# Optimization experiments

Measured on AMD Instinct MI355X. Metric: run time of the kernel, lower is better.

Reference implementation:

```python
import jax, jax.numpy as jnp
import numpy as np

N = 100000   # nodes
E = 1600000  # edges (avg degree 16)
F = 64       # num_features
H = 32       # hidden_size
C = 2        # num_classes
BN_EPS = 1e-5


def setup_inputs() -> dict:
    key = jax.random.key(0)
    ks = jax.random.split(key, 16)
    s_in = 1.0 / np.sqrt(F)
    s_h = 1.0 / np.sqrt(H)
    s_l = 1.0 / np.sqrt(3 * H)
    return {
        "x": jax.random.normal(ks[0], (N, F), jnp.float32),
        "edge_index": jax.random.randint(ks[1], (2, E), 0, N, dtype=jnp.int32),
        "edge_weights": jax.random.uniform(ks[2], (E,), jnp.float32),
        # GCNConv 1
        "W1": jax.random.uniform(ks[3], (F, H), jnp.float32, -s_in, s_in),
        "b1": jnp.zeros((H,), jnp.float32),
        "g1": jnp.ones((H,), jnp.float32),
        "be1": jnp.zeros((H,), jnp.float32),
        # GCNConv 2
        "W2": jax.random.uniform(ks[4], (H, H), jnp.float32, -s_h, s_h),
        "b2": jnp.zeros((H,), jnp.float32),
        "g2": jnp.ones((H,), jnp.float32),
        "be2": jnp.zeros((H,), jnp.float32),
        # GCNConv 3
        "W3": jax.random.uniform(ks[5], (H, H), jnp.float32, -s_h, s_h),
        "b3": jnp.zeros((H,), jnp.float32),
        "g3": jnp.ones((H,), jnp.float32),
        "be3": jnp.zeros((H,), jnp.float32),
        # Final linear: (3H -> C)
        "Wl": jax.random.uniform(ks[6], (3 * H, C), jnp.float32, -s_l, s_l),
        "bl": jax.random.uniform(ks[7], (C,), jnp.float32, -s_l, s_l),
    }


def _gcn_conv(x, W, b, row, col, w, n):
    # PyG GCNConv: h = x @ W; symmetric normalization with self-loops; scatter-add; + bias
    h = x @ W                                            # [N, H]
    deg = jax.ops.segment_sum(w, col, num_segments=n)    # [N]
    dis = jnp.where(deg > 0, jax.lax.rsqrt(deg), 0.0)    # deg^{-1/2}
    norm = dis[row] * w * dis[col]                       # [E+N]
    msg = h[row] * norm[:, None]                         # gather + normalize
    out = jax.ops.segment_sum(msg, col, num_segments=n)  # scatter-add to targets
    return out + b


def _bn(x, gamma, beta):
    # BatchNorm1d with batch statistics (biased variance), affine
    mu = x.mean(axis=0)
    var = x.var(axis=0)
    return (x - mu) * jax.lax.rsqrt(var + BN_EPS) * gamma + beta


def reference(x, edge_index, edge_weights,
              W1, b1, g1, be1,
              W2, b2, g2, be2,
              W3, b3, g3, be3,
              Wl, bl):
    n = x.shape[0]
    loops = jnp.arange(n, dtype=edge_index.dtype)
    row = jnp.concatenate([edge_index[0], loops])        # sources + self-loops
    col = jnp.concatenate([edge_index[1], loops])        # targets + self-loops
    w = jnp.concatenate([edge_weights, jnp.ones((n,), edge_weights.dtype)])

    out1 = _bn(jax.nn.relu(_gcn_conv(x, W1, b1, row, col, w, n)), g1, be1)
    out2 = _bn(jax.nn.relu(_gcn_conv(out1, W2, b2, row, col, w, n)), g2, be2)
    out3 = _bn(jax.nn.relu(_gcn_conv(out2, W3, b3, row, col, w, n)), g3, be3)

    rep = jnp.concatenate([out1, out2, out3], axis=1)    # [N, 3H]
    return rep @ Wl + bl                                 # [N, C]
```

## Files before the change

kernel.cpp:

```cpp
#include <hip/hip_runtime.h>

typedef unsigned int uint;
typedef unsigned char uchar;
typedef unsigned short ushort;
typedef unsigned long long ull;

#define F_IN 64
#define HD 32
#define NCLS 2
#define BN_EPS 1e-5f
#define SCHUNK 1024
#define NCOPY 8
#define FIX_SCALE 1073741824.0f
#define FIX_INV   9.313225746154785e-10f
#define MASK40 ((1ULL << 40) - 1)

__device__ __forceinline__ ull ld64(const int2* p) {
    return *reinterpret_cast<const ull*>(p);
}
__device__ __forceinline__ ushort f2bf(float f) {
    uint u = __float_as_uint(f);
    u = (u + 0x7FFFu + ((u >> 16) & 1u)) >> 16;
    return (ushort)u;
}
__device__ __forceinline__ float bf2f(ushort b) {
    return __uint_as_float((uint)b << 16);
}
__device__ __forceinline__ uchar f2e4(float x) {
    uint u = __float_as_uint(x);
    uint s = u & 0x80000000u;
    uint mag = u & 0x7fffffffu;
    if (mag < 0x3c800000u) return (uchar)(s >> 24);
    if (mag > 0x43e00000u) mag = 0x43e00000u;
    uint r = mag + 0x000FFFFFu + ((mag >> 20) & 1u);
    if (r > 0x43e00000u) r = 0x43e00000u;
    uint E = r >> 23;
    return (uchar)((s >> 24) | ((E - 120u) << 3) | ((r >> 20) & 7u));
}
__device__ __forceinline__ float e42f(uchar b) {
    uint s = ((uint)b & 0x80u) << 24;
    uint rest = (uint)b & 0x7fu;
    return __uint_as_float(s | ((rest << 20) + 0x3c000000u));
}

__global__ void hist64_kernel(const int* __restrict__ ei, const float* __restrict__ w,
                              ull* __restrict__ packed8, ushort* __restrict__ epos,
                              int E, int n) {
    int e = blockIdx.x * blockDim.x + threadIdx.x;
    if (e >= E) return;
    int k = blockIdx.x & (NCOPY - 1);
    int c = ei[E + e];
    ull fx = (ull)(w[e] * FIX_SCALE + 0.5f);
    ull old = atomicAdd(&packed8[(size_t)k * n + c], (1ULL << 40) | fx);
    epos[e] = (ushort)(old >> 40);
}

__global__ void scanA_kernel(const ull* __restrict__ packed8,
                             int* __restrict__ partial, float* __restrict__ dis, int n) {
    __shared__ int red[256];
    int base = blockIdx.x * SCHUNK;
    int tid = threadIdx.x;
    int s = 0;
    for (int i = tid; i < SCHUNK; i += 256) {
        int idx = base + i;
        if (idx < n) {
            int cnt = 0;
            ull fxs = 0;
#pragma unroll
            for (int k = 0; k < NCOPY; k++) {
                ull p = packed8[(size_t)k * n + idx];
                cnt += (int)(p >> 40);
                fxs += (p & MASK40);
            }
            s += cnt;
            float deg = (float)fxs * FIX_INV;
            dis[idx] = rsqrtf(deg + 1.0f);
        }
    }
    red[tid] = s;
    __syncthreads();
    for (int off = 128; off > 0; off >>= 1) {
        if (tid < off) red[tid] += red[tid + off];
        __syncthreads();
    }
    if (tid == 0) partial[blockIdx.x] = red[0];
}

__global__ void scanB_kernel(int* __restrict__ partial, int nb, int* __restrict__ offs_n) {
    __shared__ int lds[256];
    int tid = threadIdx.x;
    int v = (tid < nb) ? partial[tid] : 0;
    lds[tid] = v;
    __syncthreads();
    for (int off = 1; off < 256; off <<= 1) {
        int t = (tid >= off) ? lds[tid - off] : 0;
        __syncthreads();
        lds[tid] += t;
        __syncthreads();
    }
    if (tid < nb) partial[tid] = lds[tid] - v;
    if (tid == nb - 1) *offs_n = lds[tid];
}

__global__ void scanC_kernel(const ull* __restrict__ packed8, const int* __restrict__ partial,
                             int* __restrict__ offs, int* __restrict__ base8, int n) {
    __shared__ int lds[256];
    int tid = threadIdx.x;
    int i0 = blockIdx.x * SCHUNK + tid * 4;
    int cnt[4][NCOPY];
    int tot[4] = {0, 0, 0, 0};
#pragma unroll
    for (int t = 0; t < 4; t++) {
        int idx = i0 + t;
#pragma unroll
        for (int k = 0; k < NCOPY; k++) {
            int c = (idx < n) ? (int)(packed8[(size_t)k * n + idx] >> 40) : 0;
            cnt[t][k] = c;
            tot[t] += c;
        }
    }
    int tsum = tot[0] + tot[1] + tot[2] + tot[3];
    lds[tid] = tsum;
    __syncthreads();
    for (int off = 1; off < 256; off <<= 1) {
        int t = (tid >= off) ? lds[tid - off] : 0;
        __syncthreads();
        lds[tid] += t;
        __syncthreads();
    }
    int run = partial[blockIdx.x] + lds[tid] - tsum;
#pragma unroll
    for (int t = 0; t < 4; t++) {
        int idx = i0 + t;
        if (idx < n) {
            offs[idx] = run;
            int b = run;
#pragma unroll
            for (int k = 0; k < NCOPY; k++) {
                base8[(size_t)idx * NCOPY + k] = b;
                b += cnt[t][k];
            }
            run = b;
        }
    }
}

__global__ void fill_gemm1_kernel(const int* __restrict__ ei, const float* __restrict__ w,
                                  const int* __restrict__ base8, const ushort* __restrict__ epos,
                                  int2* __restrict__ centry, int E, int eb,
                                  const float* __restrict__ X, const float* __restrict__ W,
                                  const float* __restrict__ dis, ushort* __restrict__ Hb,
                                  float* __restrict__ statsCur, int n) {
    if ((int)blockIdx.x < eb) {
        int e = blockIdx.x * blockDim.x + threadIdx.x;
        if (e >= E) return;
        int k = blockIdx.x & (NCOPY - 1);
        int r = ei[e], c = ei[E + e];
        int pos = base8[(size_t)c * NCOPY + k] + (int)epos[e];
        centry[pos] = make_int2(r, __float_as_int(w[e]));
        return;
    }
    __shared__ float Wl[F_IN * HD];
    int gb = (int)blockIdx.x - eb;
    for (int i = threadIdx.x; i < F_IN * HD; i += blockDim.x) Wl[i] = W[i];
    if (gb == 0) {
        for (int i = threadIdx.x; i < NCOPY * 64; i += blockDim.x) statsCur[i] = 0.0f;
    }
    __syncthreads();
    int idx = gb * (int)blockDim.x + (int)threadIdx.x;
    if (idx >= n * HD) return;
    int node = idx >> 5, h = idx & 31;
    const float4* xr4 = reinterpret_cast<const float4*>(X + (size_t)node * F_IN);
    float acc = 0.0f;
#pragma unroll
    for (int q = 0; q < F_IN / 4; q++) {
        float4 v4 = xr4[q];
        float vs[4] = {v4.x, v4.y, v4.z, v4.w};
#pragma unroll
        for (int j = 0; j < 4; j++) {
            acc += vs[j] * Wl[(q * 4 + j) * HD + h];
        }
    }
    Hb[idx] = f2bf(acc * dis[node]);
}

template <bool FP8>
__global__ void gemm_bn_kernel(const float* __restrict__ X, const float* __restrict__ W,
                               const float* __restrict__ statsPrev, const float* __restrict__ g,
                               const float* __restrict__ be, const float* __restrict__ dis,
                               ushort* __restrict__ Hb, uchar* __restrict__ Hb8,
                               float* __restrict__ statsCur, int n) {
    __shared__ float Wl[HD * HD];
    __shared__ float scl[64];
    for (int i = threadIdx.x; i < HD * HD; i += blockDim.x) Wl[i] = W[i];
    if (threadIdx.x < 32) {
        int h = threadIdx.x;
        float sm = 0.f, sq = 0.f;
#pragma unroll
        for (int k = 0; k < NCOPY; k++) {
            sm += statsPrev[k * 64 + h];
            sq += statsPrev[k * 64 + 32 + h];
        }
        float invn = 1.0f / (float)n;
        float mean = sm * invn;
        float var = sq * invn - mean * mean;
        float sca = rsqrtf(var + BN_EPS) * g[h];
        scl[h] = sca;
        scl[32 + h] = be[h] - mean * sca;
    }
    if (blockIdx.x == 0) {
        for (int i = threadIdx.x; i < NCOPY * 64; i += blockDim.x) statsCur[i] = 0.0f;
    }
    __syncthreads();
    int idx = blockIdx.x * blockDim.x + threadIdx.x;
    if (idx >= n * HD) return;
    int node = idx >> 5, h = idx & 31;
    const float4* xr4 = reinterpret_cast<const float4*>(X + (size_t)node * HD);
    float acc = 0.0f;
#pragma unroll
    for (int q = 0; q < HD / 4; q++) {
        float4 v4 = xr4[q];
        float vs[4] = {v4.x, v4.y, v4.z, v4.w};
#pragma unroll
        for (int j = 0; j < 4; j++) {
            int k = q * 4 + j;
            acc += (vs[j] * scl[k] + scl[32 + k]) * Wl[k * HD + h];
        }
    }
    float v = acc * dis[node];
    if (FP8) Hb8[idx] = f2e4(v * 16.0f);
    else     Hb[idx]  = f2bf(v);
}

template <int NPW>
__global__ void aggV4n_kernel(const ushort* __restrict__ hb, const int* __restrict__ offs,
                              const int2* __restrict__ centry, const float* __restrict__ dis,
                              const float* __restrict__ bias, float* __restrict__ y,
                              float* __restrict__ stats, int n) {
    int wave = threadIdx.x >> 6, lane = threadIdx.x & 63, sub = lane >> 5, h = lane & 31;
    float bv = bias[h];
    float lsum = 0.f, lsq = 0.f;
    int base = (blockIdx.x * 4 + wave) * NPW;
    for (int t = 0; t < NPW; t++) {
        int node = base + t;
        if (node >= n) break;
        int s = offs[node], e2 = offs[node + 1];
        int len = e2 - s;
        int half = (len + 1) >> 1;
        int j    = sub ? (s + half) : s;
        int jend = sub ? e2 : (s + half);
        float dd = dis[node];
        float a0 = 0.f, a1 = 0.f, a2 = 0.f, a3 = 0.f;
        if (sub == 0) a0 = bf2f(hb[(size_t)node * HD + h]);
        for (; j + 3 < jend; j += 4) {
            ull p0 = ld64(centry + j);
            ull p1 = ld64(centry + j + 1);
            ull p2 = ld64(centry + j + 2);
            ull p3 = ld64(centry + j + 3);
            a0 += bf2f(hb[(size_t)(uint)p0 * HD + h]) * __uint_as_float((uint)(p0 >> 32));
            a1 += bf2f(hb[(size_t)(uint)p1 * HD + h]) * __uint_as_float((uint)(p1 >> 32));
            a2 += bf2f(hb[(size_t)(uint)p2 * HD + h]) * __uint_as_float((uint)(p2 >> 32));
            a3 += bf2f(hb[(size_t)(uint)p3 * HD + h]) * __uint_as_float((uint)(p3 >> 32));
        }
        for (; j < jend; j++) {
            ull p0 = ld64(centry + j);
            a0 += bf2f(hb[(size_t)(uint)p0 * HD + h]) * __uint_as_float((uint)(p0 >> 32));
        }
        a0 += a1 + a2 + a3;
        a0 += __shfl_xor(a0, 32, 64);
        float yv = fmaxf(fmaf(a0, dd, bv), 0.f);
        if (sub == 0) {
            y[(size_t)node * HD + h] = yv;
            lsum += yv; lsq += yv * yv;
        }
    }
    __shared__ float ls[4][32], lq[4][32];
    if (sub == 0) { ls[wave][h] = lsum; lq[wave][h] = lsq; }
    __syncthreads();
    if (threadIdx.x < 32) {
        int k = blockIdx.x & (NCOPY - 1);
        float a = ls[0][threadIdx.x] + ls[1][threadIdx.x] + ls[2][threadIdx.x] + ls[3][threadIdx.x];
        float b = lq[0][threadIdx.x] + lq[1][threadIdx.x] + lq[2][threadIdx.x] + lq[3][threadIdx.x];
        atomicAdd(&stats[k * 64 + threadIdx.x], a);
        atomicAdd(&stats[k * 64 + 32 + threadIdx.x], b);
    }
}

template <int NPW>
__global__ void aggV4n8_kernel(const uchar* __restrict__ hb8, const int* __restrict__ offs,
                               const int2* __restrict__ centry, const float* __restrict__ dis,
                               const float* __restrict__ bias, float* __restrict__ y,
                               float* __restrict__ stats, int n) {
    int wave = threadIdx.x >> 6, lane = threadIdx.x & 63, sub = lane >> 5, h = lane & 31;
    float bv = bias[h];
    float lsum = 0.f, lsq = 0.f;
    int base = (blockIdx.x * 4 + wave) * NPW;
    for (int t = 0; t < NPW; t++) {
        int node = base + t;
        if (node >= n) break;
        int s = offs[node], e2 = offs[node + 1];
        int len = e2 - s;
        int half = (len + 1) >> 1;
        int j    = sub ? (s + half) : s;
        int jend = sub ? e2 : (s + half);
        float dd = dis[node] * 0.0625f;
        float a0 = 0.f, a1 = 0.f, a2 = 0.f, a3 = 0.f;
        if (sub == 0) a0 = e42f(hb8[(size_t)node * HD + h]);
        for (; j + 3 < jend; j += 4) {
            ull p0 = ld64(centry + j);
            ull p1 = ld64(centry + j + 1);
            ull p2 = ld64(centry + j + 2);
            ull p3 = ld64(centry + j + 3);
            a0 += e42f(hb8[(size_t)(uint)p0 * HD + h]) * __uint_as_float((uint)(p0 >> 32));
            a1 += e42f(hb8[(size_t)(uint)p1 * HD + h]) * __uint_as_float((uint)(p1 >> 32));
            a2 += e42f(hb8[(size_t)(uint)p2 * HD + h]) * __uint_as_float((uint)(p2 >> 32));
            a3 += e42f(hb8[(size_t)(uint)p3 * HD + h]) * __uint_as_float((uint)(p3 >> 32));
        }
        for (; j < jend; j++) {
            ull p0 = ld64(centry + j);
            a0 += e42f(hb8[(size_t)(uint)p0 * HD + h]) * __uint_as_float((uint)(p0 >> 32));
        }
        a0 += a1 + a2 + a3;
        a0 += __shfl_xor(a0, 32, 64);
        float yv = fmaxf(fmaf(a0, dd, bv), 0.f);
        if (sub == 0) {
            y[(size_t)node * HD + h] = yv;
            lsum += yv; lsq += yv * yv;
        }
    }
    __shared__ float ls[4][32], lq[4][32];
    if (sub == 0) { ls[wave][h] = lsum; lq[wave][h] = lsq; }
    __syncthreads();
    if (threadIdx.x < 32) {
        int k = blockIdx.x & (NCOPY - 1);
        float a = ls[0][threadIdx.x] + ls[1][threadIdx.x] + ls[2][threadIdx.x] + ls[3][threadIdx.x];
        float b = lq[0][threadIdx.x] + lq[1][threadIdx.x] + lq[2][threadIdx.x] + lq[3][threadIdx.x];
        atomicAdd(&stats[k * 64 + threadIdx.x], a);
        atomicAdd(&stats[k * 64 + 32 + threadIdx.x], b);
    }
}

__global__ void final_kernel(const float* __restrict__ y1, const float* __restrict__ y2,
                             const float* __restrict__ y3,
                             const float* __restrict__ s1, const float* __restrict__ s2,
                             const float* __restrict__ s3,
                             const float* __restrict__ g1, const float* __restrict__ be1,
                             const float* __restrict__ g2, const float* __restrict__ be2,
                             const float* __restrict__ g3, const float* __restrict__ be3,
                             const float* __restrict__ Wl, const float* __restrict__ bl,
                             float* __restrict__ out, int n) {
    __shared__ float Ws[96 * NCLS];
    __shared__ float scs[3][64];
    __shared__ float bs[NCLS];
    for (int i = threadIdx.x; i < 96 * NCLS; i += blockDim.x) Ws[i] = Wl[i];
    if (threadIdx.x < 96) {
        int L = threadIdx.x >> 5, h = threadIdx.x & 31;
        const float* st = (L == 0) ? s1 : (L == 1) ? s2 : s3;
        const float* gg = (L == 0) ? g1 : (L == 1) ? g2 : g3;
        const float* bb = (L == 0) ? be1 : (L == 1) ? be2 : be3;
        float sm = 0.f, sq = 0.f;
#pragma unroll
        for (int k = 0; k < NCOPY; k++) {
            sm += st[k * 64 + h];
            sq += st[k * 64 + 32 + h];
        }
        float invn = 1.0f / (float)n;
        float mean = sm * invn;
        float var = sq * invn - mean * mean;
        float sca = rsqrtf(var + BN_EPS) * gg[h];
        scs[L][h] = sca;
        scs[L][32 + h] = bb[h] - mean * sca;
    }
    if (threadIdx.x < NCLS) bs[threadIdx.x] = bl[threadIdx.x];
    __syncthreads();
    int i = blockIdx.x * blockDim.x + threadIdx.x;
    if (i >= n) return;
    float a0 = bs[0], a1 = bs[1];
    const float* ys[3] = {y1 + (size_t)i * HD, y2 + (size_t)i * HD, y3 + (size_t)i * HD};
#pragma unroll
    for (int L = 0; L < 3; L++) {
        const float4* r4 = reinterpret_cast<const float4*>(ys[L]);
#pragma unroll
        for (int q = 0; q < HD / 4; q++) {
            float4 v4 = r4[q];
            float vs[4] = {v4.x, v4.y, v4.z, v4.w};
#pragma unroll
            for (int j = 0; j < 4; j++) {
                int h = q * 4 + j;
                float v = vs[j] * scs[L][h] + scs[L][32 + h];
                a0 += v * Ws[(L * 32 + h) * 2];
                a1 += v * Ws[(L * 32 + h) * 2 + 1];
            }
        }
    }
    out[(size_t)i * 2] = a0;
    out[(size_t)i * 2 + 1] = a1;
}

extern "C" void kernel_launch(void* const* d_in, const int* in_sizes, int n_in,
                              void* d_out, int out_size, void* d_ws, size_t ws_size,
                              hipStream_t stream) {
    const float* x  = (const float*)d_in[0];
    const int*   ei = (const int*)d_in[1];
    const float* ew = (const float*)d_in[2];
    const float* W1 = (const float*)d_in[3];  const float* b1  = (const float*)d_in[4];
    const float* g1 = (const float*)d_in[5];  const float* be1 = (const float*)d_in[6];
    const float* W2 = (const float*)d_in[7];  const float* b2  = (const float*)d_in[8];
    const float* g2 = (const float*)d_in[9];  const float* be2 = (const float*)d_in[10];
    const float* W3 = (const float*)d_in[11]; const float* b3  = (const float*)d_in[12];
    const float* g3 = (const float*)d_in[13]; const float* be3 = (const float*)d_in[14];
    const float* Wl = (const float*)d_in[15]; const float* bl  = (const float*)d_in[16];

    int n = in_sizes[0] / F_IN;
    int E = in_sizes[1] / 2;

    char* ws = (char*)d_ws;
    auto alloc = [&](size_t bytes) -> char* {
        char* p = ws;
        ws += (bytes + 255) / 256 * 256;
        return p;
    };
    ull*    packed8 = (ull*)alloc((size_t)NCOPY * n * 8);
    float*  dis     = (float*)alloc((size_t)n * 4);
    int*    offs    = (int*)alloc((size_t)(n + 1) * 4);
    int*    base8   = (int*)alloc((size_t)n * NCOPY * 4);
    int*    partial = (int*)alloc(256 * 4);
    ushort* epos    = (ushort*)alloc((size_t)E * 2);
    int2*   centry  = (int2*)alloc((size_t)E * 8);
    ushort* hb      = (ushort*)alloc((size_t)n * HD * 2);
    uchar*  hb8     = (uchar*)alloc((size_t)n * HD);
    float*  y1      = (float*)alloc((size_t)n * HD * 4);
    float*  y2      = (float*)alloc((size_t)n * HD * 4);
    float*  y3      = (float*)alloc((size_t)n * HD * 4);
    float*  stats1  = (float*)alloc(NCOPY * 64 * 4);
    float*  stats2  = (float*)alloc(NCOPY * 64 * 4);
    float*  stats3  = (float*)alloc(NCOPY * 64 * 4);

    hipMemsetAsync(packed8, 0, (size_t)NCOPY * n * 8, stream);

    int eb  = (E + 255) / 256;
    int nb  = (n + 255) / 256;
    int nhb = (n * HD + 255) / 256;
    int scb = (n + SCHUNK - 1) / SCHUNK;
    int agb = (n + 63) / 64;

    hist64_kernel<<<eb, 256, 0, stream>>>(ei, ew, packed8, epos, E, n);
    scanA_kernel<<<scb, 256, 0, stream>>>(packed8, partial, dis, n);
    scanB_kernel<<<1, 256, 0, stream>>>(partial, scb, offs + n);
    scanC_kernel<<<scb, 256, 0, stream>>>(packed8, partial, offs, base8, n);

    fill_gemm1_kernel<<<eb + nhb, 256, 0, stream>>>(ei, ew, base8, epos, centry, E, eb,
                                                    x, W1, dis, hb, stats1, n);

    aggV4n_kernel<16><<<agb, 256, 0, stream>>>(hb, offs, centry, dis, b1, y1, stats1, n);
    gemm_bn_kernel<true><<<nhb, 256, 0, stream>>>(y1, W2, stats1, g1, be1, dis, hb, hb8, stats2, n);
    aggV4n8_kernel<16><<<agb, 256, 0, stream>>>(hb8, offs, centry, dis, b2, y2, stats2, n);
    gemm_bn_kernel<false><<<nhb, 256, 0, stream>>>(y2, W3, stats2, g3, be3, dis, hb, hb8, stats3, n);
    aggV4n_kernel<16><<<agb, 256, 0, stream>>>(hb, offs, centry, dis, b3, y3, stats3, n);

    final_kernel<<<nb, 256, 0, stream>>>(y1, y2, y3, stats1, stats2, stats3,
                                         g1, be1, g2, be2, g3, be3, Wl, bl, (float*)d_out, n);
}
```

Measured before the change: 377.7 us.

## Drop epos array via atomic cursors, fuse scan kernels, deepen layer-3 gather unroll

The histogram kernel stops returning per-edge slot positions, which removes the 2-byte-per-edge epos write and read. The CSR fill now claims slots with atomicAdd on per-node, per-copy cursors. The single-block partial scan is folded into scanC, so each block redoes the small prefix over partials and one kernel launch goes away. The third-layer aggregation gets an 8-way unrolled gather path for more memory-level parallelism. The trade-off is extra atomics in the fill and a nondeterministic edge order within each bucket, which can change float summation order.

Result: slower. 451.3 us (+19.5%).

```diff
diff --git a/kernel.cpp b/kernel.cpp
--- a/kernel.cpp
+++ b/kernel.cpp
@@ -44,15 +44,13 @@
 }
 
 __global__ void hist64_kernel(const int* __restrict__ ei, const float* __restrict__ w,
-                              ull* __restrict__ packed8, ushort* __restrict__ epos,
-                              int E, int n) {
+                              ull* __restrict__ packed8, int E, int n) {
     int e = blockIdx.x * blockDim.x + threadIdx.x;
     if (e >= E) return;
     int k = blockIdx.x & (NCOPY - 1);
     int c = ei[E + e];
     ull fx = (ull)(w[e] * FIX_SCALE + 0.5f);
-    ull old = atomicAdd(&packed8[(size_t)k * n + c], (1ULL << 40) | fx);
-    epos[e] = (ushort)(old >> 40);
+    atomicAdd(&packed8[(size_t)k * n + c], (1ULL << 40) | fx);
 }
 
 __global__ void scanA_kernel(const ull* __restrict__ packed8,
@@ -86,10 +84,12 @@
     if (tid == 0) partial[blockIdx.x] = red[0];
 }
 
-__global__ void scanB_kernel(int* __restrict__ partial, int nb, int* __restrict__ offs_n) {
+__global__ void scanC_kernel(const ull* __restrict__ packed8, const int* __restrict__ partial,
+                             int* __restrict__ offs, int* __restrict__ cursor8, int n, int scb) {
     __shared__ int lds[256];
+    __shared__ int chunkBase, totalE;
     int tid = threadIdx.x;
-    int v = (tid < nb) ? partial[tid] : 0;
+    int v = (tid < scb) ? partial[tid] : 0;
     lds[tid] = v;
     __syncthreads();
     for (int off = 1; off < 256; off <<= 1) {
@@ -98,14 +98,11 @@
         lds[tid] += t;
         __syncthreads();
     }
-    if (tid < nb) partial[tid] = lds[tid] - v;
-    if (tid == nb - 1) *offs_n = lds[tid];
-}
-
-__global__ void scanC_kernel(const ull* __restrict__ packed8, const int* __restrict__ partial,
-                             int* __restrict__ offs, int* __restrict__ base8, int n) {
-    __shared__ int lds[256];
-    int tid = threadIdx.x;
+    if (tid == 0) {
+        chunkBase = lds[blockIdx.x] - partial[blockIdx.x];
+        totalE = lds[scb - 1];
+    }
+    __syncthreads();
     int i0 = blockIdx.x * SCHUNK + tid * 4;
     int cnt[4][NCOPY];
     int tot[4] = {0, 0, 0, 0};
@@ -128,7 +125,7 @@
         lds[tid] += t;
         __syncthreads();
     }
-    int run = partial[blockIdx.x] + lds[tid] - tsum;
+    int run = chunkBase + lds[tid] - tsum;
 #pragma unroll
     for (int t = 0; t < 4; t++) {
         int idx = i0 + t;
@@ -137,16 +134,17 @@
             int b = run;
 #pragma unroll
             for (int k = 0; k < NCOPY; k++) {
-                base8[(size_t)idx * NCOPY + k] = b;
+                cursor8[(size_t)idx * NCOPY + k] = b;
                 b += cnt[t][k];
             }
             run = b;
         }
     }
+    if (blockIdx.x == 0 && tid == 0) offs[n] = totalE;
 }
 
 __global__ void fill_gemm1_kernel(const int* __restrict__ ei, const float* __restrict__ w,
-                                  const int* __restrict__ base8, const ushort* __restrict__ epos,
+                                  int* __restrict__ cursor8,
                                   int2* __restrict__ centry, int E, int eb,
                                   const float* __restrict__ X, const float* __restrict__ W,
                                   const float* __restrict__ dis, ushort* __restrict__ Hb,
@@ -156,7 +154,7 @@
         if (e >= E) return;
         int k = blockIdx.x & (NCOPY - 1);
         int r = ei[e], c = ei[E + e];
-        int pos = base8[(size_t)c * NCOPY + k] + (int)epos[e];
+        int pos = atomicAdd(&cursor8[(size_t)c * NCOPY + k], 1);
         centry[pos] = make_int2(r, __float_as_int(w[e]));
         return;
     }
@@ -232,7 +230,7 @@
     else     Hb[idx]  = f2bf(v);
 }
 
-template <int NPW>
+template <int NPW, bool DEEP8>
 __global__ void aggV4n_kernel(const ushort* __restrict__ hb, const int* __restrict__ offs,
                               const int2* __restrict__ centry, const float* __restrict__ dis,
                               const float* __restrict__ bias, float* __restrict__ y,
@@ -252,6 +250,28 @@
         float dd = dis[node];
         float a0 = 0.f, a1 = 0.f, a2 = 0.f, a3 = 0.f;
         if (sub == 0) a0 = bf2f(hb[(size_t)node * HD + h]);
+        if (DEEP8) {
+            float a4 = 0.f, a5 = 0.f, a6 = 0.f, a7 = 0.f;
+            for (; j + 7 < jend; j += 8) {
+                ull p0 = ld64(centry + j);
+                ull p1 = ld64(centry + j + 1);
+                ull p2 = ld64(centry + j + 2);
+                ull p3 = ld64(centry + j + 3);
+                ull p4 = ld64(centry + j + 4);
+                ull p5 = ld64(centry + j + 5);
+                ull p6 = ld64(centry + j + 6);
+                ull p7 = ld64(centry + j + 7);
+                a0 += bf2f(hb[(size_t)(uint)p0 * HD + h]) * __uint_as_float((uint)(p0 >> 32));
+                a1 += bf2f(hb[(size_t)(uint)p1 * HD + h]) * __uint_as_float((uint)(p1 >> 32));
+                a2 += bf2f(hb[(size_t)(uint)p2 * HD + h]) * __uint_as_float((uint)(p2 >> 32));
+                a3 += bf2f(hb[(size_t)(uint)p3 * HD + h]) * __uint_as_float((uint)(p3 >> 32));
+                a4 += bf2f(hb[(size_t)(uint)p4 * HD + h]) * __uint_as_float((uint)(p4 >> 32));
+                a5 += bf2f(hb[(size_t)(uint)p5 * HD + h]) * __uint_as_float((uint)(p5 >> 32));
+                a6 += bf2f(hb[(size_t)(uint)p6 * HD + h]) * __uint_as_float((uint)(p6 >> 32));
+                a7 += bf2f(hb[(size_t)(uint)p7 * HD + h]) * __uint_as_float((uint)(p7 >> 32));
+            }
+            a0 += a4; a1 += a5; a2 += a6; a3 += a7;
+        }
         for (; j + 3 < jend; j += 4) {
             ull p0 = ld64(centry + j);
             ull p1 = ld64(centry + j + 1);
@@ -423,9 +443,8 @@
     ull*    packed8 = (ull*)alloc((size_t)NCOPY * n * 8);
     float*  dis     = (float*)alloc((size_t)n * 4);
     int*    offs    = (int*)alloc((size_t)(n + 1) * 4);
-    int*    base8   = (int*)alloc((size_t)n * NCOPY * 4);
+    int*    cursor8 = (int*)alloc((size_t)n * NCOPY * 4);
     int*    partial = (int*)alloc(256 * 4);
-    ushort* epos    = (ushort*)alloc((size_t)E * 2);
     int2*   centry  = (int2*)alloc((size_t)E * 8);
     ushort* hb      = (ushort*)alloc((size_t)n * HD * 2);
     uchar*  hb8     = (uchar*)alloc((size_t)n * HD);
@@ -444,19 +463,18 @@
     int scb = (n + SCHUNK - 1) / SCHUNK;
     int agb = (n + 63) / 64;
 
-    hist64_kernel<<<eb, 256, 0, stream>>>(ei, ew, packed8, epos, E, n);
+    hist64_kernel<<<eb, 256, 0, stream>>>(ei, ew, packed8, E, n);
     scanA_kernel<<<scb, 256, 0, stream>>>(packed8, partial, dis, n);
-    scanB_kernel<<<1, 256, 0, stream>>>(partial, scb, offs + n);
-    scanC_kernel<<<scb, 256, 0, stream>>>(packed8, partial, offs, base8, n);
-
-    fill_gemm1_kernel<<<eb + nhb, 256, 0, stream>>>(ei, ew, base8, epos, centry, E, eb,
+    scanC_kernel<<<scb, 256, 0, stream>>>(packed8, partial, offs, cursor8, n, scb);
+
+    fill_gemm1_kernel<<<eb + nhb, 256, 0, stream>>>(ei, ew, cursor8, centry, E, eb,
                                                     x, W1, dis, hb, stats1, n);
 
-    aggV4n_kernel<16><<<agb, 256, 0, stream>>>(hb, offs, centry, dis, b1, y1, stats1, n);
+    aggV4n_kernel<16, false><<<agb, 256, 0, stream>>>(hb, offs, centry, dis, b1, y1, stats1, n);
     gemm_bn_kernel<true><<<nhb, 256, 0, stream>>>(y1, W2, stats1, g1, be1, dis, hb, hb8, stats2, n);
     aggV4n8_kernel<16><<<agb, 256, 0, stream>>>(hb8, offs, centry, dis, b2, y2, stats2, n);
     gemm_bn_kernel<false><<<nhb, 256, 0, stream>>>(y2, W3, stats2, g3, be3, dis, hb, hb8, stats3, n);
-    aggV4n_kernel<16><<<agb, 256, 0, stream>>>(hb, offs, centry, dis, b3, y3, stats3, n);
+    aggV4n_kernel<16, true><<<agb, 256, 0, stream>>>(hb, offs, centry, dis, b3, y3, stats3, n);
 
     final_kernel<<<nb, 256, 0, stream>>>(y1, y2, y3, stats1, stats2, stats3,
                                          g1, be1, g2, be2, g3, be3, Wl, bl, (float*)d_out, n);
```
